# Performance work log

Measured on AMD Instinct MI355X. Metric: run time of the kernel, lower is better.

Reference implementation:

```python
import jax, jax.numpy as jnp
import numpy as np

D_MODEL = 1024
NUM_HEADS = 16
WINDOW = 256
HEAD_DIM = D_MODEL // NUM_HEADS


def setup_inputs() -> dict:
    key = jax.random.key(0)
    ks = jax.random.split(key, 5)
    B, L, D = 2, 2048, D_MODEL
    s = 1.0 / np.sqrt(D)
    x = jax.random.normal(ks[0], (B, L, D), dtype=jnp.float32)
    w_qkv = jax.random.normal(ks[1], (3 * D, D), dtype=jnp.float32) * s
    b_qkv = jnp.zeros((3 * D,), dtype=jnp.float32)
    w_proj = jax.random.normal(ks[2], (D, D), dtype=jnp.float32) * s
    b_proj = jnp.zeros((D,), dtype=jnp.float32)
    return {"x": x, "w_qkv": w_qkv, "b_qkv": b_qkv, "w_proj": w_proj, "b_proj": b_proj}


def reference(x, w_qkv, b_qkv, w_proj, b_proj):
    B, L, D = x.shape
    H, E = NUM_HEADS, HEAD_DIM
    scale = 1.0 / jnp.sqrt(jnp.asarray(E, dtype=x.dtype))
    # torch Linear: y = x @ W.T + b
    qkv = (x @ w_qkv.T + b_qkv).reshape(B, L, 3, H, E)
    qkv = jnp.transpose(qkv, (2, 0, 3, 1, 4))  # [3, B, H, L, E]
    q, k, v = qkv[0], qkv[1], qkv[2]
    scores = jnp.einsum('bhle,bhme->bhlm', q, k) * scale  # [B,H,L,L]
    i = jnp.arange(L)[:, None]
    j = jnp.arange(L)[None, :]
    mask = (j > i) | ((i - j) >= WINDOW)  # causal OR outside window
    scores = jnp.where(mask, jnp.asarray(-10000.0, dtype=scores.dtype), scores)
    attn = jax.nn.softmax(scores, axis=-1)
    out = jnp.einsum('bhlm,bhme->bhle', attn, v)  # [B,H,L,E]
    out = jnp.transpose(out, (0, 2, 1, 3)).reshape(B, L, D)
    return out @ w_proj.T + b_proj
```

## Files before the change

### kernel.cpp

```cpp
#include <hip/hip_runtime.h>

typedef __bf16 bf16x8 __attribute__((ext_vector_type(8)));
typedef float f32x4 __attribute__((ext_vector_type(4)));
typedef unsigned short u16;
typedef unsigned int u32;

__device__ __forceinline__ u16 f2bf(float f) {
  u32 u = __builtin_bit_cast(u32, f);
  u32 r = (u + 0x7FFFu + ((u >> 16) & 1u)) >> 16;
  return (u16)r;
}

__device__ __forceinline__ void gload16(const u16* g, u16* lds_base) {
  __builtin_amdgcn_global_load_lds(
      (const __attribute__((address_space(1))) void*)g,
      (__attribute__((address_space(3))) void*)lds_base, 16, 0, 0);
}

__global__ void cast_f32_bf16(const float* __restrict__ src, u16* __restrict__ dst, int n4) {
  int i = blockIdx.x * blockDim.x + threadIdx.x;
  int stride = gridDim.x * blockDim.x;
  const float4* s4 = (const float4*)src;
  uint2* d2 = (uint2*)dst;
  for (; i < n4; i += stride) {
    float4 f = s4[i];
    uint2 o;
    o.x = (u32)f2bf(f.x) | ((u32)f2bf(f.y) << 16);
    o.y = (u32)f2bf(f.z) | ((u32)f2bf(f.w) << 16);
    d2[i] = o;
  }
}

template<int OUT_BF16>
__global__ __launch_bounds__(256) void gemm_nt(
    const u16* __restrict__ A, const u16* __restrict__ W,
    const float* __restrict__ bias, void* __restrict__ Cout,
    int M, int N, int K)
{
  __shared__ u16 Alds[128][32];
  __shared__ u16 Blds[128][32];
  const int tid  = threadIdx.x;
  const int lane = tid & 63;
  const int wave = tid >> 6;
  const int wm = (wave >> 1) * 64;
  const int wn = (wave & 1) * 64;
  const int m0 = blockIdx.y * 128;
  const int n0 = blockIdx.x * 128;
  const int quad = lane >> 4;
  const int li   = lane & 15;

  const int srow = wave * 32 + (lane >> 2);
  const int scol = (lane & 3) * 8;
  const u16* ga = &A[(size_t)(m0 + srow) * K + scol];
  const u16* gb = &W[(size_t)(n0 + srow) * K + scol];
  u16* la = &Alds[wave * 32][0];
  u16* lb = &Blds[wave * 32][0];

  f32x4 acc[4][4] = {};

  for (int k0 = 0; k0 < K; k0 += 32) {
    __syncthreads();
#pragma unroll
    for (int i = 0; i < 2; i++) {
      gload16(ga + (size_t)i * 16 * K + k0, la + i * 16 * 32);
      gload16(gb + (size_t)i * 16 * K + k0, lb + i * 16 * 32);
    }
    __syncthreads();
    bf16x8 af[4], bfr[4];
#pragma unroll
    for (int t = 0; t < 4; t++) {
      af[t]  = *(const bf16x8*)&Alds[wm + t * 16 + li][quad * 8];
      bfr[t] = *(const bf16x8*)&Blds[wn + t * 16 + li][quad * 8];
    }
#pragma unroll
    for (int mt = 0; mt < 4; mt++)
#pragma unroll
      for (int nt = 0; nt < 4; nt++)
        acc[mt][nt] = __builtin_amdgcn_mfma_f32_16x16x32_bf16(af[mt], bfr[nt], acc[mt][nt], 0, 0, 0);
  }

#pragma unroll
  for (int mt = 0; mt < 4; mt++)
#pragma unroll
    for (int nt = 0; nt < 4; nt++) {
      int gn = n0 + wn + nt * 16 + li;
      float bv = bias[gn];
#pragma unroll
      for (int r = 0; r < 4; r++) {
        int gm = m0 + wm + mt * 16 + quad * 4 + r;
        float v = acc[mt][nt][r] + bv;
        if (OUT_BF16)
          ((u16*)Cout)[(size_t)gm * N + gn] = f2bf(v);
        else
          ((float*)Cout)[(size_t)gm * N + gn] = v;
      }
    }
}

__global__ __launch_bounds__(256) void attn_kernel(const u16* __restrict__ qkv,
                                                   u16* __restrict__ aout)
{
  const int L = 2048, DQ = 3072, D = 1024;
  const int q0 = blockIdx.x * 64;
  const int h  = blockIdx.y;
  const int b  = blockIdx.z;
  const int tid  = threadIdx.x;
  const int lane = tid & 63;
  const int wave = tid >> 6;
  const int quad = lane >> 4;
  const int li   = lane & 15;

  __shared__ u16 Klds[64][68];
  __shared__ u16 Vlds[64][68];
  __shared__ u16 Plds[4][16][68];

  const u16* base = qkv + (size_t)b * L * DQ + h * 64;

  bf16x8 qf[2];
  {
    const u16* qsrc = base + (size_t)(q0 + wave * 16 + li) * DQ;
    qf[0] = *(const bf16x8*)&qsrc[quad * 8];
    qf[1] = *(const bf16x8*)&qsrc[32 + quad * 8];
  }

  f32x4 O[4] = {};
  float mrow[4], lrow[4];
#pragma unroll
  for (int r = 0; r < 4; r++) { mrow[r] = -1e30f; lrow[r] = 0.f; }

  const float scale = 0.125f;
  const int gq = q0 + wave * 16 + quad * 4;

  for (int t = 0; t < 5; t++) {
    int kb = q0 - 256 + t * 64;
    if (kb < 0) continue;
    __syncthreads();
    {
      int r = tid >> 3, c = (tid & 7) * 8;
      const u16* ks = base + D + (size_t)kb * DQ;
      const u16* vs = base + 2 * D + (size_t)kb * DQ;
      *(uint4*)&Klds[r][c]      = *(const uint4*)&ks[(size_t)r * DQ + c];
      *(uint4*)&Klds[r + 32][c] = *(const uint4*)&ks[(size_t)(r + 32) * DQ + c];
      *(uint4*)&Vlds[r][c]      = *(const uint4*)&vs[(size_t)r * DQ + c];
      *(uint4*)&Vlds[r + 32][c] = *(const uint4*)&vs[(size_t)(r + 32) * DQ + c];
    }
    __syncthreads();

    f32x4 sacc[4] = {};
#pragma unroll
    for (int nt = 0; nt < 4; nt++) {
      bf16x8 kf0 = *(const bf16x8*)&Klds[nt * 16 + li][quad * 8];
      bf16x8 kf1 = *(const bf16x8*)&Klds[nt * 16 + li][32 + quad * 8];
      sacc[nt] = __builtin_amdgcn_mfma_f32_16x16x32_bf16(qf[0], kf0, sacc[nt], 0, 0, 0);
      sacc[nt] = __builtin_amdgcn_mfma_f32_16x16x32_bf16(qf[1], kf1, sacc[nt], 0, 0, 0);
    }

    float p[4][4];
    float rmax[4];
#pragma unroll
    for (int r = 0; r < 4; r++) rmax[r] = -1e30f;
#pragma unroll
    for (int nt = 0; nt < 4; nt++) {
      int gj = kb + nt * 16 + li;
#pragma unroll
      for (int r = 0; r < 4; r++) {
        bool masked = (gj > gq + r) || ((gq + r) - gj >= 256);
        float s = masked ? -1e30f : sacc[nt][r] * scale;
        p[nt][r] = s;
        rmax[r] = fmaxf(rmax[r], s);
      }
    }
#pragma unroll
    for (int d = 1; d < 16; d <<= 1)
#pragma unroll
      for (int r = 0; r < 4; r++)
        rmax[r] = fmaxf(rmax[r], __shfl_xor(rmax[r], d, 64));

    float alpha[4];
#pragma unroll
    for (int r = 0; r < 4; r++) {
      float mn = fmaxf(mrow[r], rmax[r]);
      alpha[r] = __expf(mrow[r] - mn);
      mrow[r] = mn;
    }
    float lsum[4] = {0.f, 0.f, 0.f, 0.f};
#pragma unroll
    for (int nt = 0; nt < 4; nt++)
#pragma unroll
      for (int r = 0; r < 4; r++) {
        float s = p[nt][r];
        float pv = (s > -1e29f) ? __expf(s - mrow[r]) : 0.f;
        p[nt][r] = pv;
        lsum[r] += pv;
      }
#pragma unroll
    for (int d = 1; d < 16; d <<= 1)
#pragma unroll
      for (int r = 0; r < 4; r++)
        lsum[r] += __shfl_xor(lsum[r], d, 64);
#pragma unroll
    for (int r = 0; r < 4; r++) lrow[r] = lrow[r] * alpha[r] + lsum[r];

#pragma unroll
    for (int nt = 0; nt < 4; nt++)
#pragma unroll
      for (int r = 0; r < 4; r++)
        Plds[wave][quad * 4 + r][nt * 16 + li] = f2bf(p[nt][r]);

#pragma unroll
    for (int nt = 0; nt < 4; nt++)
#pragma unroll
      for (int r = 0; r < 4; r++) O[nt][r] *= alpha[r];

    bf16x8 pf0 = *(const bf16x8*)&Plds[wave][li][quad * 8];
    bf16x8 pf1 = *(const bf16x8*)&Plds[wave][li][32 + quad * 8];
#pragma unroll
    for (int nt = 0; nt < 4; nt++) {
      union { u16 u[8]; bf16x8 v; } vb0, vb1;
#pragma unroll
      for (int j = 0; j < 8; j++) {
        vb0.u[j] = Vlds[quad * 8 + j][nt * 16 + li];
        vb1.u[j] = Vlds[32 + quad * 8 + j][nt * 16 + li];
      }
      O[nt] = __builtin_amdgcn_mfma_f32_16x16x32_bf16(pf0, vb0.v, O[nt], 0, 0, 0);
      O[nt] = __builtin_amdgcn_mfma_f32_16x16x32_bf16(pf1, vb1.v, O[nt], 0, 0, 0);
    }
  }

#pragma unroll
  for (int r = 0; r < 4; r++) {
    float inv = 1.f / lrow[r];
#pragma unroll
    for (int nt = 0; nt < 4; nt++)
      aout[(size_t)(b * L + gq + r) * D + h * 64 + nt * 16 + li] = f2bf(O[nt][r] * inv);
  }
}

extern "C" void kernel_launch(void* const* d_in, const int* in_sizes, int n_in,
                              void* d_out, int out_size, void* d_ws, size_t ws_size,
                              hipStream_t stream) {
  const float* x      = (const float*)d_in[0];
  const float* w_qkv  = (const float*)d_in[1];
  const float* b_qkv  = (const float*)d_in[2];
  const float* w_proj = (const float*)d_in[3];
  const float* b_proj = (const float*)d_in[4];
  float* out = (float*)d_out;

  char* ws = (char*)d_ws;
  u16* x_bf     = (u16*)(ws);
  u16* wqkv_bf  = (u16*)(ws + ((size_t)8  << 20));
  u16* wproj_bf = (u16*)(ws + ((size_t)14 << 20));
  u16* qkv_bf   = (u16*)(ws + ((size_t)16 << 20));
  u16* attn_bf  = (u16*)(ws + ((size_t)40 << 20));

  cast_f32_bf16<<<1024, 256, 0, stream>>>(x,      x_bf,     (2 * 2048 * 1024) / 4);
  cast_f32_bf16<<<1024, 256, 0, stream>>>(w_qkv,  wqkv_bf,  (3072 * 1024) / 4);
  cast_f32_bf16<<<512,  256, 0, stream>>>(w_proj, wproj_bf, (1024 * 1024) / 4);

  gemm_nt<1><<<dim3(3072 / 128, 4096 / 128), 256, 0, stream>>>(
      x_bf, wqkv_bf, b_qkv, qkv_bf, 4096, 3072, 1024);

  attn_kernel<<<dim3(2048 / 64, 16, 2), 256, 0, stream>>>(qkv_bf, attn_bf);

  gemm_nt<0><<<dim3(1024 / 128, 4096 / 128), 256, 0, stream>>>(
      attn_bf, wproj_bf, b_proj, out, 4096, 1024, 1024);
}
```

Measured before the change: 177.2 us.

## Fuse casts, double K-step in GEMM, narrow proj tiles, transpose V in LDS

The three cast launches become one combined kernel. The GEMM now processes K in steps of 64, using two LDS sub-tiles per barrier pair, which halves the synchronisation count. The output-projection GEMM uses 128x64 tiles so that more blocks fill the CUs. The attention kernel stores V transposed in LDS so the PV operands can be read as 16-byte vectors instead of eight scalar loads each, at the cost of scattered scalar writes when staging V.

```diff
diff --git a/kernel.cpp b/kernel.cpp
--- a/kernel.cpp
+++ b/kernel.cpp
@@ -17,72 +17,86 @@
       (__attribute__((address_space(3))) void*)lds_base, 16, 0, 0);
 }
 
-__global__ void cast_f32_bf16(const float* __restrict__ src, u16* __restrict__ dst, int n4) {
+__global__ void cast_all(const float* __restrict__ x,  u16* __restrict__ xo,
+                         const float* __restrict__ wq, u16* __restrict__ wqo,
+                         const float* __restrict__ wp, u16* __restrict__ wpo) {
+  const int NX = (2 * 2048 * 1024) / 4;
+  const int NQ = (3072 * 1024) / 4;
+  const int NP = (1024 * 1024) / 4;
   int i = blockIdx.x * blockDim.x + threadIdx.x;
   int stride = gridDim.x * blockDim.x;
-  const float4* s4 = (const float4*)src;
-  uint2* d2 = (uint2*)dst;
-  for (; i < n4; i += stride) {
-    float4 f = s4[i];
+  for (; i < NX + NQ + NP; i += stride) {
+    const float4* s; uint2* d; int j;
+    if (i < NX)            { s = (const float4*)x;  d = (uint2*)xo;  j = i; }
+    else if (i < NX + NQ)  { s = (const float4*)wq; d = (uint2*)wqo; j = i - NX; }
+    else                   { s = (const float4*)wp; d = (uint2*)wpo; j = i - NX - NQ; }
+    float4 f = s[j];
     uint2 o;
     o.x = (u32)f2bf(f.x) | ((u32)f2bf(f.y) << 16);
     o.y = (u32)f2bf(f.z) | ((u32)f2bf(f.w) << 16);
-    d2[i] = o;
-  }
-}
-
-template<int OUT_BF16>
+    d[j] = o;
+  }
+}
+
+template<int OUT_BF16, int BM, int BN>
 __global__ __launch_bounds__(256) void gemm_nt(
     const u16* __restrict__ A, const u16* __restrict__ W,
     const float* __restrict__ bias, void* __restrict__ Cout,
     int M, int N, int K)
 {
-  __shared__ u16 Alds[128][32];
-  __shared__ u16 Blds[128][32];
+  constexpr int NT = BN / 32;
+  __shared__ u16 Alds[2][BM][32];
+  __shared__ u16 Blds[2][BN][32];
   const int tid  = threadIdx.x;
   const int lane = tid & 63;
   const int wave = tid >> 6;
   const int wm = (wave >> 1) * 64;
-  const int wn = (wave & 1) * 64;
-  const int m0 = blockIdx.y * 128;
-  const int n0 = blockIdx.x * 128;
+  const int wn = (wave & 1) * (BN / 2);
+  const int m0 = blockIdx.y * BM;
+  const int n0 = blockIdx.x * BN;
   const int quad = lane >> 4;
   const int li   = lane & 15;
 
-  const int srow = wave * 32 + (lane >> 2);
-  const int scol = (lane & 3) * 8;
-  const u16* ga = &A[(size_t)(m0 + srow) * K + scol];
-  const u16* gb = &W[(size_t)(n0 + srow) * K + scol];
-  u16* la = &Alds[wave * 32][0];
-  u16* lb = &Blds[wave * 32][0];
-
-  f32x4 acc[4][4] = {};
-
-  for (int k0 = 0; k0 < K; k0 += 32) {
-    __syncthreads();
-#pragma unroll
-    for (int i = 0; i < 2; i++) {
-      gload16(ga + (size_t)i * 16 * K + k0, la + i * 16 * 32);
-      gload16(gb + (size_t)i * 16 * K + k0, lb + i * 16 * 32);
-    }
-    __syncthreads();
-    bf16x8 af[4], bfr[4];
-#pragma unroll
-    for (int t = 0; t < 4; t++) {
-      af[t]  = *(const bf16x8*)&Alds[wm + t * 16 + li][quad * 8];
-      bfr[t] = *(const bf16x8*)&Blds[wn + t * 16 + li][quad * 8];
-    }
-#pragma unroll
-    for (int mt = 0; mt < 4; mt++)
-#pragma unroll
-      for (int nt = 0; nt < 4; nt++)
-        acc[mt][nt] = __builtin_amdgcn_mfma_f32_16x16x32_bf16(af[mt], bfr[nt], acc[mt][nt], 0, 0, 0);
+  const u16* ga = &A[(size_t)(m0 + wave * (BM / 4) + (lane >> 2)) * K + (lane & 3) * 8];
+  const u16* gb = &W[(size_t)(n0 + wave * (BN / 4) + (lane >> 2)) * K + (lane & 3) * 8];
+
+  f32x4 acc[4][NT] = {};
+
+  for (int k0 = 0; k0 < K; k0 += 64) {
+    __syncthreads();
+#pragma unroll
+    for (int ks = 0; ks < 2; ks++) {
+#pragma unroll
+      for (int i = 0; i < BM / 64; i++)
+        gload16(ga + (size_t)i * 16 * K + k0 + ks * 32,
+                &Alds[ks][wave * (BM / 4) + i * 16][0]);
+#pragma unroll
+      for (int i = 0; i < BN / 64; i++)
+        gload16(gb + (size_t)i * 16 * K + k0 + ks * 32,
+                &Blds[ks][wave * (BN / 4) + i * 16][0]);
+    }
+    __syncthreads();
+#pragma unroll
+    for (int ks = 0; ks < 2; ks++) {
+      bf16x8 af[4], bfr[NT];
+#pragma unroll
+      for (int t = 0; t < 4; t++)
+        af[t] = *(const bf16x8*)&Alds[ks][wm + t * 16 + li][quad * 8];
+#pragma unroll
+      for (int t = 0; t < NT; t++)
+        bfr[t] = *(const bf16x8*)&Blds[ks][wn + t * 16 + li][quad * 8];
+#pragma unroll
+      for (int mt = 0; mt < 4; mt++)
+#pragma unroll
+        for (int nt = 0; nt < NT; nt++)
+          acc[mt][nt] = __builtin_amdgcn_mfma_f32_16x16x32_bf16(af[mt], bfr[nt], acc[mt][nt], 0, 0, 0);
+    }
   }
 
 #pragma unroll
   for (int mt = 0; mt < 4; mt++)
 #pragma unroll
-    for (int nt = 0; nt < 4; nt++) {
+    for (int nt = 0; nt < NT; nt++) {
       int gn = n0 + wn + nt * 16 + li;
       float bv = bias[gn];
 #pragma unroll
@@ -111,7 +125,7 @@
   const int li   = lane & 15;
 
   __shared__ u16 Klds[64][68];
-  __shared__ u16 Vlds[64][68];
+  __shared__ u16 Vt[64][68];
   __shared__ u16 Plds[4][16][68];
 
   const u16* base = qkv + (size_t)b * L * DQ + h * 64;
@@ -141,8 +155,14 @@
       const u16* vs = base + 2 * D + (size_t)kb * DQ;
       *(uint4*)&Klds[r][c]      = *(const uint4*)&ks[(size_t)r * DQ + c];
       *(uint4*)&Klds[r + 32][c] = *(const uint4*)&ks[(size_t)(r + 32) * DQ + c];
-      *(uint4*)&Vlds[r][c]      = *(const uint4*)&vs[(size_t)r * DQ + c];
-      *(uint4*)&Vlds[r + 32][c] = *(const uint4*)&vs[(size_t)(r + 32) * DQ + c];
+      __align__(16) u16 v0[8], v1[8];
+      *(uint4*)v0 = *(const uint4*)&vs[(size_t)r * DQ + c];
+      *(uint4*)v1 = *(const uint4*)&vs[(size_t)(r + 32) * DQ + c];
+#pragma unroll
+      for (int j = 0; j < 8; j++) {
+        Vt[c + j][r]      = v0[j];
+        Vt[c + j][r + 32] = v1[j];
+      }
     }
     __syncthreads();
 
@@ -216,14 +236,10 @@
     bf16x8 pf1 = *(const bf16x8*)&Plds[wave][li][32 + quad * 8];
 #pragma unroll
     for (int nt = 0; nt < 4; nt++) {
-      union { u16 u[8]; bf16x8 v; } vb0, vb1;
-#pragma unroll
-      for (int j = 0; j < 8; j++) {
-        vb0.u[j] = Vlds[quad * 8 + j][nt * 16 + li];
-        vb1.u[j] = Vlds[32 + quad * 8 + j][nt * 16 + li];
-      }
-      O[nt] = __builtin_amdgcn_mfma_f32_16x16x32_bf16(pf0, vb0.v, O[nt], 0, 0, 0);
-      O[nt] = __builtin_amdgcn_mfma_f32_16x16x32_bf16(pf1, vb1.v, O[nt], 0, 0, 0);
+      bf16x8 vb0 = *(const bf16x8*)&Vt[nt * 16 + li][quad * 8];
+      bf16x8 vb1 = *(const bf16x8*)&Vt[nt * 16 + li][32 + quad * 8];
+      O[nt] = __builtin_amdgcn_mfma_f32_16x16x32_bf16(pf0, vb0, O[nt], 0, 0, 0);
+      O[nt] = __builtin_amdgcn_mfma_f32_16x16x32_bf16(pf1, vb1, O[nt], 0, 0, 0);
     }
   }
 
@@ -253,15 +269,13 @@
   u16* qkv_bf   = (u16*)(ws + ((size_t)16 << 20));
   u16* attn_bf  = (u16*)(ws + ((size_t)40 << 20));
 
-  cast_f32_bf16<<<1024, 256, 0, stream>>>(x,      x_bf,     (2 * 2048 * 1024) / 4);
-  cast_f32_bf16<<<1024, 256, 0, stream>>>(w_qkv,  wqkv_bf,  (3072 * 1024) / 4);
-  cast_f32_bf16<<<512,  256, 0, stream>>>(w_proj, wproj_bf, (1024 * 1024) / 4);
-
-  gemm_nt<1><<<dim3(3072 / 128, 4096 / 128), 256, 0, stream>>>(
+  cast_all<<<1024, 256, 0, stream>>>(x, x_bf, w_qkv, wqkv_bf, w_proj, wproj_bf);
+
+  gemm_nt<1, 128, 128><<<dim3(3072 / 128, 4096 / 128), 256, 0, stream>>>(
       x_bf, wqkv_bf, b_qkv, qkv_bf, 4096, 3072, 1024);
 
   attn_kernel<<<dim3(2048 / 64, 16, 2), 256, 0, stream>>>(qkv_bf, attn_bf);
 
-  gemm_nt<0><<<dim3(1024 / 128, 4096 / 128), 256, 0, stream>>>(
+  gemm_nt<0, 128, 64><<<dim3(1024 / 64, 4096 / 128), 256, 0, stream>>>(
       attn_bf, wproj_bf, b_proj, out, 4096, 1024, 1024);
 }
```

New measurement: 175.2 us. No clear change (-1.1%).
